# Optimization experiments

Measured on AMD Instinct MI355X. Metric: run time of the kernel, lower is better.

## Reference

```python
import jax, jax.numpy as jnp
import numpy as np

B, L, S, H, E, D = 2, 2048, 2048, 16, 64, 64


def setup_inputs() -> dict:
    key = jax.random.key(0)
    ks = jax.random.split(key, 6)
    return {
        "q1": jax.random.normal(ks[0], (B, L, H, E), dtype=jnp.float32),
        "k1": jax.random.normal(ks[1], (B, S, H, E), dtype=jnp.float32),
        "v1": jax.random.normal(ks[2], (B, S, H, D), dtype=jnp.float32),
        "q2": jax.random.normal(ks[3], (B, L, H, E), dtype=jnp.float32),
        "k2": jax.random.normal(ks[4], (B, S, H, E), dtype=jnp.float32),
        "v2": jax.random.normal(ks[5], (B, S, H, D), dtype=jnp.float32),
        "attn_mask": 0,  # accepted but unused by the original forward
    }


def reference(q1, k1, v1, q2, k2, v2, attn_mask):
    # scale = 1/sqrt(E) (self.scale is None in init_kwargs)
    scale = 1.0 / jnp.sqrt(jnp.asarray(q1.shape[-1], dtype=q1.dtype))
    # dual QK scores: [B,H,L,S]
    scores1 = jnp.einsum('blhe,bshe->bhls', q1, k1)
    scores2 = jnp.einsum('blhe,bshe->bhls', q2, k2)
    # eval-mode (dropout disabled for deterministic reference)
    A = jnp.tanh(scores1 * scale) * jax.nn.sigmoid(scores2 * scale)
    # weighted V matmul: [B,L,H,D]
    out = jnp.einsum('bhls,bshd->blhd', A, v1)
    return out
```

## Files before the change

### kernel.cpp

```cpp
#include <hip/hip_runtime.h>

constexpr int Bc = 2, Lc = 2048, Sc = 2048, Hc = 16, Ec = 64, Dc = 64;
constexpr int TILES = Sc / 64;
constexpr int NBH   = Bc * Hc;
constexpr size_t TILE_ELEMS = 4096;
constexpr size_t ARR_ELEMS  = (size_t)NBH * TILES * TILE_ELEMS;
constexpr size_t WS_NEED    = ARR_ELEMS * 2 * 3;

typedef float          f32x4  __attribute__((ext_vector_type(4)));
typedef float          f32x16 __attribute__((ext_vector_type(16)));
typedef __bf16         bf16x8 __attribute__((ext_vector_type(8)));
typedef unsigned short u16x8  __attribute__((ext_vector_type(8)));
typedef unsigned short u16x4  __attribute__((ext_vector_type(4)));
typedef unsigned int   u32x4  __attribute__((ext_vector_type(4)));

extern "C" __device__ float __ocml_native_exp2_f32(float);

static __device__ __forceinline__ unsigned cvtpk(float lo, float hi) {
    unsigned r;
    asm("v_cvt_pk_bf16_f32 %0, %1, %2" : "=v"(r) : "v"(lo), "v"(hi));
    return r;
}

static __device__ __forceinline__ float fexp2(float x) {
    return __ocml_native_exp2_f32(x);
}

__global__ __launch_bounds__(256) void prepass_kernel(
    const float* __restrict__ k1, const float* __restrict__ k2,
    const float* __restrict__ v1,
    unsigned short* __restrict__ k1b, unsigned short* __restrict__ k2b,
    unsigned short* __restrict__ vb)
{
    __shared__ unsigned short vt[64 * 80];

    const int blk = blockIdx.x;
    const int st  = blk & 31;
    const int bh  = blk >> 5;
    const int b   = bh >> 4, h = bh & 15;
    const int s0  = st * 64;
    const size_t tileo = (size_t)blk * TILE_ELEMS;

    #pragma unroll
    for (int it = 0; it < 2; ++it) {
        int u  = threadIdx.x + it * 256;
        int s  = u >> 3, e8 = u & 7;
        size_t g = ((size_t)((b * Sc + s0 + s) * Hc + h)) * Ec + e8 * 8;

        float4 x0 = *reinterpret_cast<const float4*>(k1 + g);
        float4 x1 = *reinterpret_cast<const float4*>(k1 + g + 4);
        u32x4 o;
        o[0] = cvtpk(x0.x, x0.y); o[1] = cvtpk(x0.z, x0.w);
        o[2] = cvtpk(x1.x, x1.y); o[3] = cvtpk(x1.z, x1.w);
        *reinterpret_cast<u32x4*>(&k1b[tileo + (size_t)(e8 * 64 + s) * 8]) = o;

        x0 = *reinterpret_cast<const float4*>(k2 + g);
        x1 = *reinterpret_cast<const float4*>(k2 + g + 4);
        o[0] = cvtpk(x0.x, x0.y); o[1] = cvtpk(x0.z, x0.w);
        o[2] = cvtpk(x1.x, x1.y); o[3] = cvtpk(x1.z, x1.w);
        *reinterpret_cast<u32x4*>(&k2b[tileo + (size_t)(e8 * 64 + s) * 8]) = o;

        x0 = *reinterpret_cast<const float4*>(v1 + g);
        x1 = *reinterpret_cast<const float4*>(v1 + g + 4);
        o[0] = cvtpk(x0.x, x0.y); o[1] = cvtpk(x0.z, x0.w);
        o[2] = cvtpk(x1.x, x1.y); o[3] = cvtpk(x1.z, x1.w);
        *reinterpret_cast<u32x4*>(&vt[s * 80 + e8 * 8]) = o;
    }
    __syncthreads();

    #pragma unroll
    for (int it = 0; it < 2; ++it) {
        int u  = threadIdx.x + it * 256;
        int d  = u >> 3, sc8 = u & 7;
        u16x8 o;
        #pragma unroll
        for (int j = 0; j < 8; ++j) o[j] = vt[(sc8 * 8 + j) * 80 + d];
        *reinterpret_cast<u16x8*>(&vb[tileo + (size_t)(sc8 * 64 + d) * 8]) = o;
    }
}

__global__ __launch_bounds__(256, 3) void fused_kernel(
    const float* __restrict__ q1, const float* __restrict__ q2,
    const unsigned short* __restrict__ k1b, const unsigned short* __restrict__ k2b,
    const unsigned short* __restrict__ vb, float* __restrict__ out)
{
    __shared__ float mbuf[4 * 1280];

    const int orig    = blockIdx.x;
    const int logical = (orig & 7) * 128 + (orig >> 3);
    const int lblk = logical & 31;
    const int bh   = logical >> 5;
    const int b    = bh >> 4, h = bh & 15;

    const int tid  = threadIdx.x;
    const int w    = tid >> 6;
    const int lane = tid & 63;
    const int l31  = lane & 31;
    const int hi   = lane >> 5;
    const int qsub = w >> 1;
    const int sh   = w & 1;

    constexpr float C1 = 0.36067376022224085f;
    constexpr float C2 = -0.18033688011112043f;
    const int    qrow  = lblk * 64 + qsub * 32 + l31;
    const size_t qbase = ((size_t)((b * Lc + qrow) * Hc + h)) * Ec;
    u32x4 qa1[4], qa2[4];
    #pragma unroll
    for (int es = 0; es < 4; ++es) {
        const float* p1 = q1 + qbase + es * 16 + hi * 8;
        const float* p2 = q2 + qbase + es * 16 + hi * 8;
        float4 x0 = *reinterpret_cast<const float4*>(p1);
        float4 x1 = *reinterpret_cast<const float4*>(p1 + 4);
        qa1[es] = (u32x4){cvtpk(x0.x * C1, x0.y * C1), cvtpk(x0.z * C1, x0.w * C1),
                          cvtpk(x1.x * C1, x1.y * C1), cvtpk(x1.z * C1, x1.w * C1)};
        x0 = *reinterpret_cast<const float4*>(p2);
        x1 = *reinterpret_cast<const float4*>(p2 + 4);
        qa2[es] = (u32x4){cvtpk(x0.x * C2, x0.y * C2), cvtpk(x0.z * C2, x0.w * C2),
                          cvtpk(x1.x * C2, x1.y * C2), cvtpk(x1.z * C2, x1.w * C2)};
    }

    f32x16 acc0 = {}, acc1 = {};

    const unsigned short* k1g = k1b + (size_t)bh * TILES * TILE_ELEMS;
    const unsigned short* k2g = k2b + (size_t)bh * TILES * TILE_ELEMS;
    const unsigned short* vg  = vb  + (size_t)bh * TILES * TILE_ELEMS;

    const int srow = sh * 32 + l31;
    int koff[4];
    #pragma unroll
    for (int es = 0; es < 4; ++es)
        koff[es] = ((es * 2 + hi) * 64 + srow) * 8;

    int voff[4];
    #pragma unroll
    for (int dt = 0; dt < 2; ++dt)
        #pragma unroll
        for (int ks = 0; ks < 2; ++ks)
            voff[dt * 2 + ks] = ((sh * 4 + ks * 2 + hi) * 64 + dt * 32 + l31) * 8;

    for (int st = 0; st < TILES; ++st) {
        const unsigned short* kt1 = k1g + (size_t)st * TILE_ELEMS;
        const unsigned short* kt2 = k2g + (size_t)st * TILE_ELEMS;
        const unsigned short* vt  = vg  + (size_t)st * TILE_ELEMS;

        u16x8 kf1[4], kf2[4];
        #pragma unroll
        for (int es = 0; es < 4; ++es) {
            kf1[es] = *reinterpret_cast<const u16x8*>(&kt1[koff[es]]);
            kf2[es] = *reinterpret_cast<const u16x8*>(&kt2[koff[es]]);
        }
        u16x8 vfr[4];
        #pragma unroll
        for (int i = 0; i < 4; ++i)
            vfr[i] = *reinterpret_cast<const u16x8*>(&vt[voff[i]]);

        f32x16 s1a = {}, s2a = {};
        #pragma unroll
        for (int es = 0; es < 4; ++es) {
            s1a = __builtin_amdgcn_mfma_f32_32x32x16_bf16(
                __builtin_bit_cast(bf16x8, kf1[es]), __builtin_bit_cast(bf16x8, qa1[es]), s1a, 0, 0, 0);
            s2a = __builtin_amdgcn_mfma_f32_32x32x16_bf16(
                __builtin_bit_cast(bf16x8, kf2[es]), __builtin_bit_cast(bf16x8, qa2[es]), s2a, 0, 0, 0);
        }

        float p[16];
        #pragma unroll
        for (int i = 0; i < 16; ++i) {
            float t  = fexp2(s1a[i]);
            float uu = fexp2(s2a[i]);
            p[i] = (t - 1.f) * __builtin_amdgcn_rcpf((t + 1.f) * (1.f + uu));
        }

        #pragma unroll
        for (int ks = 0; ks < 2; ++ks) {
            unsigned A0 = cvtpk(p[8 * ks + 0], p[8 * ks + 1]);
            unsigned A1 = cvtpk(p[8 * ks + 2], p[8 * ks + 3]);
            unsigned B0 = cvtpk(p[8 * ks + 4], p[8 * ks + 5]);
            unsigned B1 = cvtpk(p[8 * ks + 6], p[8 * ks + 7]);
            asm("v_permlane32_swap_b32 %0, %1" : "+v"(A0), "+v"(B0));
            asm("v_permlane32_swap_b32 %0, %1" : "+v"(A1), "+v"(B1));
            bf16x8 pa = __builtin_bit_cast(bf16x8, (u32x4){A0, A1, B0, B1});
            acc0 = __builtin_amdgcn_mfma_f32_32x32x16_bf16(pa, __builtin_bit_cast(bf16x8, vfr[ks]),     acc0, 0, 0, 0);
            acc1 = __builtin_amdgcn_mfma_f32_32x32x16_bf16(pa, __builtin_bit_cast(bf16x8, vfr[2 + ks]), acc1, 0, 0, 0);
        }
    }

    __syncthreads();
    if (sh == 1) {
        #pragma unroll
        for (int r4 = 0; r4 < 4; ++r4) {
            *reinterpret_cast<f32x4*>(&mbuf[(qsub * 2 + 0) * 1280 + lane * 20 + r4 * 4]) =
                (f32x4){acc0[r4 * 4 + 0], acc0[r4 * 4 + 1], acc0[r4 * 4 + 2], acc0[r4 * 4 + 3]};
            *reinterpret_cast<f32x4*>(&mbuf[(qsub * 2 + 1) * 1280 + lane * 20 + r4 * 4]) =
                (f32x4){acc1[r4 * 4 + 0], acc1[r4 * 4 + 1], acc1[r4 * 4 + 2], acc1[r4 * 4 + 3]};
        }
    }
    __syncthreads();
    if (sh == 0) {
        #pragma unroll
        for (int dt = 0; dt < 2; ++dt) {
            float m[16];
            #pragma unroll
            for (int r4 = 0; r4 < 4; ++r4) {
                f32x4 v = *reinterpret_cast<const f32x4*>(&mbuf[(qsub * 2 + dt) * 1280 + lane * 20 + r4 * 4]);
                m[r4 * 4 + 0] = v[0]; m[r4 * 4 + 1] = v[1]; m[r4 * 4 + 2] = v[2]; m[r4 * 4 + 3] = v[3];
            }
            #pragma unroll
            for (int r = 0; r < 16; ++r) {
                float val = m[r] + (dt == 0 ? acc0[r] : acc1[r]);
                int q = lblk * 64 + qsub * 32 + (r & 3) + 8 * (r >> 2) + 4 * hi;
                out[((size_t)(b * Lc + q) * Hc + h) * Dc + dt * 32 + l31] = val;
            }
        }
    }
}

static __device__ __forceinline__ unsigned short f2bf(float f) {
    unsigned u = __builtin_bit_cast(unsigned, f);
    u += 0x7fffu + ((u >> 16) & 1u);
    return (unsigned short)(u >> 16);
}

__global__ __launch_bounds__(256) void fallback_kernel(
    const float* __restrict__ q1, const float* __restrict__ k1,
    const float* __restrict__ v1, const float* __restrict__ q2,
    const float* __restrict__ k2, float* __restrict__ out)
{
    constexpr int KSTR = 72, VSTR = 88, PSTR = 88;
    __shared__ unsigned short k1t[64 * KSTR];
    __shared__ unsigned short k2t[64 * KSTR];
    __shared__ unsigned short vtt[64 * VSTR];
    __shared__ unsigned short pt [4 * 16 * PSTR];

    const int blk  = blockIdx.x;
    const int lblk = blk & 31;
    const int bh   = blk >> 5;
    const int b    = bh >> 4;
    const int h    = bh & 15;
    const int tid  = threadIdx.x;
    const int w    = tid >> 6;
    const int lane = tid & 63;
    const int lr   = lane & 15;
    const int lg   = lane >> 4;

    const int    qrow  = lblk * 64 + w * 16 + lr;
    const size_t qbase = ((size_t)(b * Lc + qrow) * Hc + h) * Ec;
    bf16x8 a1[2], a2[2];
    for (int es = 0; es < 2; ++es) {
        u16x8 t1, t2;
        for (int j = 0; j < 8; ++j) {
            t1[j] = f2bf(q1[qbase + es * 32 + lg * 8 + j]);
            t2[j] = f2bf(q2[qbase + es * 32 + lg * 8 + j]);
        }
        a1[es] = __builtin_bit_cast(bf16x8, t1);
        a2[es] = __builtin_bit_cast(bf16x8, t2);
    }
    f32x4 acc[4];
    for (int i = 0; i < 4; ++i) acc[i] = (f32x4){0.f, 0.f, 0.f, 0.f};
    constexpr float CT = 0.25f, CS = -0.125f;

    for (int s0 = 0; s0 < Sc; s0 += 64) {
        for (int it = 0; it < 4; ++it) {
            int idx = tid + it * 256;
            int sr  = idx >> 4;
            int c4  = (idx & 15) << 2;
            size_t gk = ((size_t)(b * Sc + s0 + sr) * Hc + h) * Ec + c4;
            float4 x1 = *reinterpret_cast<const float4*>(k1 + gk);
            float4 x2 = *reinterpret_cast<const float4*>(k2 + gk);
            float4 xv = *reinterpret_cast<const float4*>(v1 + gk);
            u16x4 o1, o2;
            o1[0]=f2bf(x1.x); o1[1]=f2bf(x1.y); o1[2]=f2bf(x1.z); o1[3]=f2bf(x1.w);
            o2[0]=f2bf(x2.x); o2[1]=f2bf(x2.y); o2[2]=f2bf(x2.z); o2[3]=f2bf(x2.w);
            *reinterpret_cast<u16x4*>(&k1t[sr * KSTR + c4]) = o1;
            *reinterpret_cast<u16x4*>(&k2t[sr * KSTR + c4]) = o2;
            vtt[(c4 + 0) * VSTR + sr] = f2bf(xv.x);
            vtt[(c4 + 1) * VSTR + sr] = f2bf(xv.y);
            vtt[(c4 + 2) * VSTR + sr] = f2bf(xv.z);
            vtt[(c4 + 3) * VSTR + sr] = f2bf(xv.w);
        }
        __syncthreads();
        for (int ct = 0; ct < 4; ++ct) {
            f32x4 s1 = {0.f,0.f,0.f,0.f}, s2 = {0.f,0.f,0.f,0.f};
            for (int es = 0; es < 2; ++es) {
                bf16x8 b1 = __builtin_bit_cast(bf16x8,
                    *reinterpret_cast<const u16x8*>(&k1t[(ct*16 + lr) * KSTR + es*32 + lg*8]));
                bf16x8 b2 = __builtin_bit_cast(bf16x8,
                    *reinterpret_cast<const u16x8*>(&k2t[(ct*16 + lr) * KSTR + es*32 + lg*8]));
                s1 = __builtin_amdgcn_mfma_f32_16x16x32_bf16(a1[es], b1, s1, 0, 0, 0);
                s2 = __builtin_amdgcn_mfma_f32_16x16x32_bf16(a2[es], b2, s2, 0, 0, 0);
            }
            for (int i = 0; i < 4; ++i) {
                float xa = fminf(fmaxf(s1[i] * CT, -30.f), 30.f);
                float xb = fminf(fmaxf(s2[i] * CS, -30.f), 30.f);
                float t  = __expf(xa);
                float u  = __expf(xb);
                float p  = (t - 1.f) * __builtin_amdgcn_rcpf((t + 1.f) * (1.f + u));
                pt[(w*16 + lg*4 + i) * PSTR + ct*16 + lr] = f2bf(p);
            }
        }
        asm volatile("s_waitcnt lgkmcnt(0)" ::: "memory");
        for (int ks = 0; ks < 2; ++ks) {
            bf16x8 pa = __builtin_bit_cast(bf16x8,
                *reinterpret_cast<const u16x8*>(&pt[(w*16 + lr) * PSTR + ks*32 + lg*8]));
            for (int dt = 0; dt < 4; ++dt) {
                bf16x8 vf = __builtin_bit_cast(bf16x8,
                    *reinterpret_cast<const u16x8*>(&vtt[(dt*16 + lr) * VSTR + ks*32 + lg*8]));
                acc[dt] = __builtin_amdgcn_mfma_f32_16x16x32_bf16(pa, vf, acc[dt], 0, 0, 0);
            }
        }
        __syncthreads();
    }
    const int orow = lblk * 64 + w * 16;
    for (int dt = 0; dt < 4; ++dt)
        for (int i = 0; i < 4; ++i) {
            int l = orow + lg * 4 + i;
            out[((size_t)(b * Lc + l) * Hc + h) * Dc + dt * 16 + lr] = acc[dt][i];
        }
}

extern "C" void kernel_launch(void* const* d_in, const int* in_sizes, int n_in,
                              void* d_out, int out_size, void* d_ws, size_t ws_size,
                              hipStream_t stream) {
    const float* q1 = (const float*)d_in[0];
    const float* k1 = (const float*)d_in[1];
    const float* v1 = (const float*)d_in[2];
    const float* q2 = (const float*)d_in[3];
    const float* k2 = (const float*)d_in[4];
    float* out = (float*)d_out;

    if (ws_size >= WS_NEED) {
        unsigned short* k1b = (unsigned short*)d_ws;
        unsigned short* k2b = k1b + ARR_ELEMS;
        unsigned short* vbp = k2b + ARR_ELEMS;
        prepass_kernel<<<dim3(NBH * TILES), dim3(256), 0, stream>>>(k1, k2, v1, k1b, k2b, vbp);
        fused_kernel<<<dim3(NBH * TILES), dim3(256), 0, stream>>>(q1, q2, k1b, k2b, vbp, out);
    } else {
        fallback_kernel<<<dim3(NBH * TILES), dim3(256), 0, stream>>>(q1, k1, v1, q2, k2, out);
    }
}
```

Before: 116.4 us.

## Raise occupancy to 4 waves, serialize QK passes, batch reciprocals, add MFMA priority hints

Launch bounds go from 3 to 4 blocks per CU, which forces a tighter register budget. To fit it, the K1 and K2 score passes now run one after the other through a single K fragment buffer, and tanh's exp is computed before the K2 loads. The per-element reciprocal is replaced by one rcp per four elements using products of denominators. The MFMA sections get s_setprio hints and pointer increments replace per-iteration offset arithmetic. The cost is less overlap between the two QK chains and possible register spilling under the tighter bound.

```diff
diff --git a/kernel.cpp b/kernel.cpp
--- a/kernel.cpp
+++ b/kernel.cpp
@@ -79,7 +79,7 @@
     }
 }
 
-__global__ __launch_bounds__(256, 3) void fused_kernel(
+__global__ __launch_bounds__(256, 4) void fused_kernel(
     const float* __restrict__ q1, const float* __restrict__ q2,
     const unsigned short* __restrict__ k1b, const unsigned short* __restrict__ k2b,
     const unsigned short* __restrict__ vb, float* __restrict__ out)
@@ -121,68 +121,90 @@
 
     f32x16 acc0 = {}, acc1 = {};
 
-    const unsigned short* k1g = k1b + (size_t)bh * TILES * TILE_ELEMS;
-    const unsigned short* k2g = k2b + (size_t)bh * TILES * TILE_ELEMS;
-    const unsigned short* vg  = vb  + (size_t)bh * TILES * TILE_ELEMS;
-
-    const int srow = sh * 32 + l31;
-    int koff[4];
-    #pragma unroll
-    for (int es = 0; es < 4; ++es)
-        koff[es] = ((es * 2 + hi) * 64 + srow) * 8;
-
-    int voff[4];
-    #pragma unroll
-    for (int dt = 0; dt < 2; ++dt)
-        #pragma unroll
-        for (int ks = 0; ks < 2; ++ks)
-            voff[dt * 2 + ks] = ((sh * 4 + ks * 2 + hi) * 64 + dt * 32 + l31) * 8;
+    const int srow  = sh * 32 + l31;
+    const int kofs0 = (hi * 64 + srow) * 8;
+    const int vofs0 = ((sh * 4 + hi) * 64 + l31) * 8;
+
+    const unsigned short* kt1 = k1b + (size_t)bh * TILES * TILE_ELEMS + kofs0;
+    const unsigned short* kt2 = k2b + (size_t)bh * TILES * TILE_ELEMS + kofs0;
+    const unsigned short* vt  = vb  + (size_t)bh * TILES * TILE_ELEMS + vofs0;
 
     for (int st = 0; st < TILES; ++st) {
-        const unsigned short* kt1 = k1g + (size_t)st * TILE_ELEMS;
-        const unsigned short* kt2 = k2g + (size_t)st * TILE_ELEMS;
-        const unsigned short* vt  = vg  + (size_t)st * TILE_ELEMS;
-
-        u16x8 kf1[4], kf2[4];
-        #pragma unroll
-        for (int es = 0; es < 4; ++es) {
-            kf1[es] = *reinterpret_cast<const u16x8*>(&kt1[koff[es]]);
-            kf2[es] = *reinterpret_cast<const u16x8*>(&kt2[koff[es]]);
-        }
+        u16x8 kf[4];
+        #pragma unroll
+        for (int es = 0; es < 4; ++es)
+            kf[es] = *reinterpret_cast<const u16x8*>(kt1 + es * 1024);
+
+        f32x16 s1a = {};
+        __builtin_amdgcn_s_setprio(1);
+        #pragma unroll
+        for (int es = 0; es < 4; ++es)
+            s1a = __builtin_amdgcn_mfma_f32_32x32x16_bf16(
+                __builtin_bit_cast(bf16x8, kf[es]),
+                __builtin_bit_cast(bf16x8, qa1[es]), s1a, 0, 0, 0);
+        __builtin_amdgcn_s_setprio(0);
+
+        float tt[16];
+        #pragma unroll
+        for (int i = 0; i < 16; ++i) tt[i] = fexp2(s1a[i]);
+
+        #pragma unroll
+        for (int es = 0; es < 4; ++es)
+            kf[es] = *reinterpret_cast<const u16x8*>(kt2 + es * 1024);
+
+        f32x16 s2a = {};
+        __builtin_amdgcn_s_setprio(1);
+        #pragma unroll
+        for (int es = 0; es < 4; ++es)
+            s2a = __builtin_amdgcn_mfma_f32_32x32x16_bf16(
+                __builtin_bit_cast(bf16x8, kf[es]),
+                __builtin_bit_cast(bf16x8, qa2[es]), s2a, 0, 0, 0);
+        __builtin_amdgcn_s_setprio(0);
+
         u16x8 vfr[4];
         #pragma unroll
-        for (int i = 0; i < 4; ++i)
-            vfr[i] = *reinterpret_cast<const u16x8*>(&vt[voff[i]]);
-
-        f32x16 s1a = {}, s2a = {};
-        #pragma unroll
-        for (int es = 0; es < 4; ++es) {
-            s1a = __builtin_amdgcn_mfma_f32_32x32x16_bf16(
-                __builtin_bit_cast(bf16x8, kf1[es]), __builtin_bit_cast(bf16x8, qa1[es]), s1a, 0, 0, 0);
-            s2a = __builtin_amdgcn_mfma_f32_32x32x16_bf16(
-                __builtin_bit_cast(bf16x8, kf2[es]), __builtin_bit_cast(bf16x8, qa2[es]), s2a, 0, 0, 0);
-        }
-
-        float p[16];
-        #pragma unroll
-        for (int i = 0; i < 16; ++i) {
-            float t  = fexp2(s1a[i]);
-            float uu = fexp2(s2a[i]);
-            p[i] = (t - 1.f) * __builtin_amdgcn_rcpf((t + 1.f) * (1.f + uu));
-        }
-
+        for (int dt = 0; dt < 2; ++dt)
+            #pragma unroll
+            for (int ks = 0; ks < 2; ++ks)
+                vfr[dt * 2 + ks] = *reinterpret_cast<const u16x8*>(vt + dt * 256 + ks * 1024);
+
+        unsigned pw[8];
+        #pragma unroll
+        for (int c = 0; c < 4; ++c) {
+            float dn[4], p[4];
+            #pragma unroll
+            for (int j = 0; j < 4; ++j) {
+                float u = fexp2(s2a[4 * c + j]);
+                dn[j] = __builtin_fmaf(tt[4 * c + j], u, tt[4 * c + j]) + (u + 1.f);
+            }
+            float d01 = dn[0] * dn[1];
+            float d23 = dn[2] * dn[3];
+            float inv = __builtin_amdgcn_rcpf(d01 * d23);
+            float i01 = inv * d23, i23 = inv * d01;
+            p[0] = (tt[4 * c + 0] - 1.f) * (dn[1] * i01);
+            p[1] = (tt[4 * c + 1] - 1.f) * (dn[0] * i01);
+            p[2] = (tt[4 * c + 2] - 1.f) * (dn[3] * i23);
+            p[3] = (tt[4 * c + 3] - 1.f) * (dn[2] * i23);
+            pw[2 * c]     = cvtpk(p[0], p[1]);
+            pw[2 * c + 1] = cvtpk(p[2], p[3]);
+        }
+
+        __builtin_amdgcn_s_setprio(1);
         #pragma unroll
         for (int ks = 0; ks < 2; ++ks) {
-            unsigned A0 = cvtpk(p[8 * ks + 0], p[8 * ks + 1]);
-            unsigned A1 = cvtpk(p[8 * ks + 2], p[8 * ks + 3]);
-            unsigned B0 = cvtpk(p[8 * ks + 4], p[8 * ks + 5]);
-            unsigned B1 = cvtpk(p[8 * ks + 6], p[8 * ks + 7]);
+            unsigned A0 = pw[4 * ks + 0];
+            unsigned A1 = pw[4 * ks + 1];
+            unsigned B0 = pw[4 * ks + 2];
+            unsigned B1 = pw[4 * ks + 3];
             asm("v_permlane32_swap_b32 %0, %1" : "+v"(A0), "+v"(B0));
             asm("v_permlane32_swap_b32 %0, %1" : "+v"(A1), "+v"(B1));
             bf16x8 pa = __builtin_bit_cast(bf16x8, (u32x4){A0, A1, B0, B1});
             acc0 = __builtin_amdgcn_mfma_f32_32x32x16_bf16(pa, __builtin_bit_cast(bf16x8, vfr[ks]),     acc0, 0, 0, 0);
             acc1 = __builtin_amdgcn_mfma_f32_32x32x16_bf16(pa, __builtin_bit_cast(bf16x8, vfr[2 + ks]), acc1, 0, 0, 0);
         }
+        __builtin_amdgcn_s_setprio(0);
+
+        kt1 += TILE_ELEMS; kt2 += TILE_ELEMS; vt += TILE_ELEMS;
     }
 
     __syncthreads();
```

New measurement: 116.0 us. No clear change (-0.3%).
